# Performance work log

Hardware: AMD Instinct MI355X
Metric: run time of the kernel (lower is better)

Reference implementation:

```python
import jax, jax.numpy as jnp
import numpy as np

D_MODEL = 768
N_HEADS = 12
D_HEAD = D_MODEL // N_HEADS
D_FF = 3072
EPS = 1e-5


def setup_inputs() -> dict:
    key = jax.random.key(0)
    ks = jax.random.split(key, 12)
    s = 0.02
    return {
        "x": jax.random.normal(ks[0], (2, 2048, D_MODEL), dtype=jnp.float32),
        "ln1_g": jnp.ones((D_MODEL,), jnp.float32),
        "ln1_b": jnp.zeros((D_MODEL,), jnp.float32),
        "ln2_g": jnp.ones((D_MODEL,), jnp.float32),
        "ln2_b": jnp.zeros((D_MODEL,), jnp.float32),
        "w_qkv": jax.random.normal(ks[1], (D_MODEL, 3 * D_MODEL), jnp.float32) * s,
        "b_qkv": jnp.zeros((3 * D_MODEL,), jnp.float32),
        "w_out": jax.random.normal(ks[2], (D_MODEL, D_MODEL), jnp.float32) * s,
        "b_out": jnp.zeros((D_MODEL,), jnp.float32),
        "w_fc1": jax.random.normal(ks[3], (D_MODEL, D_FF), jnp.float32) * s,
        "b_fc1": jnp.zeros((D_FF,), jnp.float32),
        "w_fc2": jax.random.normal(ks[4], (D_FF, D_MODEL), jnp.float32) * s,
        "b_fc2": jnp.zeros((D_MODEL,), jnp.float32),
    }


def _layernorm(x, g, b):
    mu = jnp.mean(x, axis=-1, keepdims=True)
    var = jnp.var(x, axis=-1, keepdims=True)
    return (x - mu) * jax.lax.rsqrt(var + EPS) * g + b


def _attention(h, w_qkv, b_qkv, w_out, b_out):
    B, S, _ = h.shape
    qkv = h @ w_qkv + b_qkv  # [B,S,3D]
    qkv = qkv.reshape(B, S, 3, N_HEADS, D_HEAD)
    q, k, v = qkv[:, :, 0], qkv[:, :, 1], qkv[:, :, 2]  # [B,S,H,Dh]
    scale = 1.0 / np.sqrt(D_HEAD).astype(np.float32)
    scores = jnp.einsum("bqhd,bkhd->bhqk", q, k) * scale
    causal = jnp.tril(jnp.ones((S, S), bool))
    scores = jnp.where(causal[None, None], scores, -jnp.inf)
    attn = jax.nn.softmax(scores, axis=-1)
    out = jnp.einsum("bhqk,bkhd->bqhd", attn, v).reshape(B, S, D_MODEL)
    return out @ w_out + b_out


def reference(x, ln1_g, ln1_b, ln2_g, ln2_b, w_qkv, b_qkv, w_out, b_out,
              w_fc1, b_fc1, w_fc2, b_fc2):
    # x = x + Attention(LN1(x))
    x = x + _attention(_layernorm(x, ln1_g, ln1_b), w_qkv, b_qkv, w_out, b_out)
    # x = x + FFN(LN2(x)); GELU is exact (erf) to match torch nn.GELU default
    h = _layernorm(x, ln2_g, ln2_b)
    h = jax.nn.gelu(h @ w_fc1 + b_fc1, approximate=False) @ w_fc2 + b_fc2
    return x + h
```

## Files before the change

### kernel.cpp

```cpp
#include <hip/hip_runtime.h>
#include <hip/hip_bf16.h>

typedef unsigned short u16;
typedef unsigned int u32;
typedef unsigned char u8;
using short8 = __attribute__((ext_vector_type(8))) short;
using short4v = __attribute__((ext_vector_type(4))) short;
using f32x4  = __attribute__((ext_vector_type(4))) float;
using float4v = __attribute__((ext_vector_type(4))) float;

__device__ __forceinline__ u16 f2bf(float f) {
    __hip_bfloat16 h = __float2bfloat16(f);
    union { __hip_bfloat16 h; u16 u; } cv; cv.h = h; return cv.u;
}
__device__ __forceinline__ float bf2f(u16 u) {
    union { u32 u; float f; } cv; cv.u = ((u32)u) << 16; return cv.f;
}
__device__ __forceinline__ u16 f2bf_trunc(float f) {
    union { float f; u32 u; } cv; cv.f = f; return (u16)(cv.u >> 16);
}

__device__ __forceinline__ void gload_lds16(const void* g, void* l) {
    __builtin_amdgcn_global_load_lds(
        (const __attribute__((address_space(1))) u32*)g,
        (__attribute__((address_space(3))) u32*)l, 16, 0, 0);
}

__device__ __forceinline__ int xcd_remap(int flat, int nwg) {
    int q = nwg >> 3, r = nwg & 7;
    int xcd = flat & 7, pos = flat >> 3;
    int start = xcd < r ? xcd * (q + 1) : r * (q + 1) + (xcd - r) * q;
    return start + pos;
}

__global__ __launch_bounds__(256) void transpose_all(const float* __restrict__ Wq,
                                                     const float* __restrict__ Wo,
                                                     const float* __restrict__ Wf1,
                                                     const float* __restrict__ Wf2,
                                                     u16* __restrict__ Tq,
                                                     u16* __restrict__ To,
                                                     u16* __restrict__ Tf1,
                                                     u16* __restrict__ Tf2) {
    __shared__ float tile[32][33];
    int id = blockIdx.x;
    const float* W; u16* Wt; int K, N, local;
    if (id < 1728)      { W = Wq;  Wt = Tq;  K = 768;  N = 2304; local = id; }
    else if (id < 2304) { W = Wo;  Wt = To;  K = 768;  N = 768;  local = id - 1728; }
    else if (id < 4608) { W = Wf1; Wt = Tf1; K = 768;  N = 3072; local = id - 2304; }
    else                { W = Wf2; Wt = Tf2; K = 3072; N = 768;  local = id - 4608; }
    int bx = N >> 5;
    int n0 = (local % bx) * 32, k0 = (local / bx) * 32;
    int tx = threadIdx.x & 31, ty = threadIdx.x >> 5;
    for (int i = 0; i < 4; i++) {
        int k = ty + i * 8;
        tile[k][tx] = W[(long)(k0 + k) * N + n0 + tx];
    }
    __syncthreads();
    for (int i = 0; i < 4; i++) {
        int n = ty + i * 8;
        Wt[(long)(n0 + n) * K + k0 + tx] = f2bf(tile[tx][n]);
    }
}

__global__ __launch_bounds__(256) void transpose_v(const u16* __restrict__ qkv,
                                                   u16* __restrict__ Vt) {
    __shared__ u16 tile[64][72];
    int s0 = blockIdx.x * 64;
    int bh = blockIdx.y;
    int b = bh / 12, h = bh % 12;
    int tid = threadIdx.x;
    const u16* src = qkv + (long)b * 2048 * 2304 + 1536 + h * 64;
    #pragma unroll
    for (int j = 0; j < 2; ++j) {
        int c = tid + j * 256;
        int srow = c >> 3, ch = c & 7;
        *(short8*)&tile[srow][ch * 8] = *(const short8*)(src + (long)(s0 + srow) * 2304 + ch * 8);
    }
    __syncthreads();
    u16* dst = Vt + (long)bh * 64 * 2048 + s0;
    #pragma unroll
    for (int j = 0; j < 2; ++j) {
        int c = tid + j * 256;
        int d = c >> 3, ch = c & 7;
        short8 v;
        #pragma unroll
        for (int e = 0; e < 8; ++e) v[e] = (short)tile[ch * 8 + e][d];
        *(short8*)(dst + (long)d * 2048 + ch * 8) = v;
    }
}

__global__ __launch_bounds__(256) void ln_kernel(const float* __restrict__ x,
                                                 const float* __restrict__ gain,
                                                 const float* __restrict__ beta,
                                                 u16* __restrict__ out) {
    int row = blockIdx.x;
    const float* xr = x + (long)row * 768;
    int tid = threadIdx.x;
    float v[3];
    float s = 0.f, s2 = 0.f;
    for (int j = 0; j < 3; j++) {
        v[j] = xr[tid + 256 * j];
        s += v[j]; s2 += v[j] * v[j];
    }
    for (int off = 32; off; off >>= 1) {
        s  += __shfl_down(s, off);
        s2 += __shfl_down(s2, off);
    }
    __shared__ float ws[8];
    int lane = tid & 63, w = tid >> 6;
    if (lane == 0) { ws[w] = s; ws[4 + w] = s2; }
    __syncthreads();
    s  = ws[0] + ws[1] + ws[2] + ws[3];
    s2 = ws[4] + ws[5] + ws[6] + ws[7];
    float mu  = s * (1.f / 768.f);
    float var = s2 * (1.f / 768.f) - mu * mu;
    float rs  = rsqrtf(var + 1e-5f);
    for (int j = 0; j < 3; j++) {
        int c = tid + 256 * j;
        out[(long)row * 768 + c] = f2bf((v[j] - mu) * rs * gain[c] + beta[c]);
    }
}

template <int EPI>
__global__ __launch_bounds__(256) void gemm_bf16(const u16* __restrict__ A, int lda,
                                                 const u16* __restrict__ Bt, int ldb,
                                                 const float* __restrict__ bias,
                                                 const float* __restrict__ res,
                                                 void* __restrict__ Cout0,
                                                 void* __restrict__ Cout1,
                                                 int M, int N, int K, int nN) {
    __shared__ alignas(16) u16 As[3][128 * 32];
    __shared__ alignas(16) u16 Bs[3][128 * 32];
    int nwg = gridDim.x;
    int wgid = xcd_remap(blockIdx.x, nwg);
    int tN = (wgid % nN) * 128, tM = (wgid / nN) * 128;
    int z = blockIdx.z;
    const u16* Ab = A + (long)z * K;
    const u16* Bb = Bt + (long)z * K;
    void* Cw = z ? Cout1 : Cout0;
    int tid = threadIdx.x;
    int wid = tid >> 6, lane = tid & 63;
    int wm = wid >> 1, wn = wid & 1;
    int g = lane >> 4, r = lane & 15;
    int srow = tid >> 2;
    int scol = tid & 3;

    f32x4 acc[4][4] = {};
    int KT = K >> 5;

    auto stage = [&](int kt, int buf) {
        int k0 = kt << 5;
        u16* ab = As[buf];
        u16* bb = Bs[buf];
        #pragma unroll
        for (int j = 0; j < 2; ++j) {
            int row = j * 64 + srow;
            int slot = scol ^ (row & 3);
            gload_lds16(Ab + (long)(tM + row) * lda + k0 + slot * 8, ab + (j * 64 + wid * 16) * 32);
            gload_lds16(Bb + (long)(tN + row) * ldb + k0 + slot * 8, bb + (j * 64 + wid * 16) * 32);
        }
    };

    stage(0, 0);
    stage(1, 1);
    int sb = 2, cb = 0;
    for (int kt = 0; kt < KT; ++kt) {
        if (kt + 2 < KT) {
            stage(kt + 2, sb);
            if (++sb == 3) sb = 0;
            asm volatile("s_waitcnt vmcnt(8)" ::: "memory");
        } else if (kt + 1 < KT) {
            asm volatile("s_waitcnt vmcnt(4)" ::: "memory");
        } else {
            asm volatile("s_waitcnt vmcnt(0)" ::: "memory");
        }
        __builtin_amdgcn_sched_barrier(0);
        __builtin_amdgcn_s_barrier();
        const u16* ab = As[cb];
        const u16* bb = Bs[cb];
        if (++cb == 3) cb = 0;

        short8 af[4], bf[4];
        #pragma unroll
        for (int mi = 0; mi < 4; ++mi) {
            int row = wm * 64 + mi * 16 + r;
            af[mi] = *(const short8*)(ab + row * 32 + ((g ^ (row & 3)) * 8));
        }
        #pragma unroll
        for (int ni = 0; ni < 4; ++ni) {
            int row = wn * 64 + ni * 16 + r;
            bf[ni] = *(const short8*)(bb + row * 32 + ((g ^ (row & 3)) * 8));
        }
        #pragma unroll
        for (int mi = 0; mi < 4; ++mi)
            #pragma unroll
            for (int ni = 0; ni < 4; ++ni)
                acc[mi][ni] = __builtin_amdgcn_mfma_f32_16x16x32_bf16(af[mi], bf[ni], acc[mi][ni], 0, 0, 0);
        __builtin_amdgcn_s_barrier();
    }

    #pragma unroll
    for (int mi = 0; mi < 4; mi++) {
        #pragma unroll
        for (int ni = 0; ni < 4; ni++) {
            int col = tN + wn * 64 + ni * 16 + r;
            float bv = (EPI == 3) ? 0.f : bias[col];
            #pragma unroll
            for (int reg = 0; reg < 4; reg++) {
                int row = tM + wm * 64 + mi * 16 + g * 4 + reg;
                float v = acc[mi][ni][reg] + bv;
                if (EPI == 1) {
                    v += res[(long)row * N + col];
                    ((float*)Cw)[(long)row * N + col] = v;
                } else if (EPI == 2) {
                    v = 0.5f * v * (1.f + erff(v * 0.70710678118f));
                    ((u16*)Cw)[(long)row * N + col] = f2bf(v);
                } else if (EPI == 3) {
                    ((u16*)Cw)[(long)row * N + col] = f2bf(v);
                } else {
                    ((u16*)Cw)[(long)row * N + col] = f2bf(v);
                }
            }
        }
    }
}

__global__ __launch_bounds__(192) void fc2_combine(const u16* __restrict__ P0,
                                                   const u16* __restrict__ P1,
                                                   const float* __restrict__ bias,
                                                   const float* __restrict__ res,
                                                   float* __restrict__ out) {
    long row = blockIdx.x;
    int c = threadIdx.x * 4;
    long i = row * 768 + c;
    short4v a = *(const short4v*)(P0 + i);
    short4v b = *(const short4v*)(P1 + i);
    float4v bs = *(const float4v*)(bias + c);
    float4v rr = *(const float4v*)(res + i);
    float4v o;
    #pragma unroll
    for (int j = 0; j < 4; ++j)
        o[j] = bf2f((u16)a[j]) + bf2f((u16)b[j]) + bs[j] + rr[j];
    *(float4v*)(out + i) = o;
}

__device__ __constant__ u8 SLOT_QI[40] = {
    15,15,15,15, 14,14,14, 13,13,13, 12,12,12, 11,11,11, 10,10, 9,9, 8,8, 7,7, 6, 5, 4, 3,
    14,10,6,2,  13,9,5,1,  12,8,4,0 };
__device__ __constant__ u8 SLOT_C[40] = {
    0,1,2,3, 0,1,2, 0,1,2, 0,1,2, 0,1,2, 0,1, 0,1, 0,1, 0,1, 0, 0, 0, 0,
    3,2,1,0, 3,2,1,0, 3,2,1,0 };

__global__ __launch_bounds__(256) void attn_kernel(const u16* __restrict__ qkv,
                                                   const u16* __restrict__ Vt,
                                                   u16* __restrict__ Opart,
                                                   float* __restrict__ Ml) {
    __shared__ alignas(16) u16 Ks[2 * 64 * 64];
    __shared__ alignas(16) u16 Vs[2 * 64 * 64];
    __shared__ alignas(16) u16 Ps[4 * 16 * 64];
    int flat = blockIdx.x;
    int s = flat / 24, bh = flat % 24;
    int qi = SLOT_QI[s], c = SLOT_C[s];
    int b = bh / 12, h = bh % 12;
    int tid = threadIdx.x;
    int w = tid >> 6, lane = tid & 63;
    int g = lane >> 4, r = lane & 15;
    int qt0 = qi * 128;
    int qw0 = qt0 + w * 32;
    int kvbase = c * 512;
    int nit = (c < (qi >> 2)) ? 8 : (2 * (qi & 3) + 2);
    const u16* base = qkv + (long)b * 2048 * 2304;
    const u16* Qb = base + h * 64;
    const u16* Kb = base + 768 + h * 64;
    const u16* Vtb = Vt + (long)bh * 64 * 2048;

    const float SC = 0.125f * 1.44269504f;
    short8 qf[2][2];
    #pragma unroll
    for (int fi = 0; fi < 2; ++fi) {
        const u16* qrow = Qb + (long)(qw0 + fi * 16 + r) * 2304;
        qf[fi][0] = *(const short8*)(qrow + 8 * g);
        qf[fi][1] = *(const short8*)(qrow + 32 + 8 * g);
        #pragma unroll
        for (int kh = 0; kh < 2; ++kh)
            #pragma unroll
            for (int j = 0; j < 8; ++j)
                qf[fi][kh][j] = (short)f2bf(bf2f((u16)qf[fi][kh][j]) * SC);
    }

    f32x4 oacc[2][4] = {};
    float mrow[2][4], psum[2][4];
    #pragma unroll
    for (int fi = 0; fi < 2; ++fi)
        #pragma unroll
        for (int i = 0; i < 4; i++) { mrow[fi][i] = 8.0f; psum[fi][i] = 0.f; }

    auto stage = [&](int kt) {
        int kv0 = kvbase + kt * 64;
        u16* kb = Ks + (kt & 1) * 4096;
        u16* vb = Vs + (kt & 1) * 4096;
        #pragma unroll
        for (int j = 0; j < 2; ++j) {
            int cc = w * 128 + j * 64 + lane;
            int row = cc >> 3;
            int slot = (cc & 7) ^ (row & 7);
            gload_lds16(Kb + (long)(kv0 + row) * 2304 + slot * 8, kb + (w * 128 + j * 64) * 8);
            gload_lds16(Vtb + (long)row * 2048 + kv0 + slot * 8, vb + (w * 128 + j * 64) * 8);
        }
    };

    stage(0);
    for (int kt = 0; kt < nit; ++kt) {
        int kv0 = kvbase + kt * 64;
        if (kt + 1 < nit) {
            stage(kt + 1);
            asm volatile("s_waitcnt vmcnt(4)" ::: "memory");
        } else {
            asm volatile("s_waitcnt vmcnt(0)" ::: "memory");
        }
        __builtin_amdgcn_sched_barrier(0);
        __builtin_amdgcn_s_barrier();
        const u16* kb = Ks + (kt & 1) * 4096;
        const u16* vb = Vs + (kt & 1) * 4096;

        bool act0 = kv0 <= qw0 + 15;
        bool act1 = kv0 <= qw0 + 31;

        f32x4 sc[2][4] = {};
        if (act1) {
            __builtin_amdgcn_s_setprio(1);
            #pragma unroll
            for (int nt = 0; nt < 4; ++nt)
                #pragma unroll
                for (int kh = 0; kh < 2; ++kh) {
                    short8 bk = *(const short8*)(kb + (nt * 16 + r) * 64 + ((kh * 32 + g * 8) ^ ((r & 7) << 3)));
                    sc[1][nt] = __builtin_amdgcn_mfma_f32_16x16x32_bf16(qf[1][kh], bk, sc[1][nt], 0, 0, 0);
                    if (act0)
                        sc[0][nt] = __builtin_amdgcn_mfma_f32_16x16x32_bf16(qf[0][kh], bk, sc[0][nt], 0, 0, 0);
                }
            __builtin_amdgcn_s_setprio(0);

            #pragma unroll
            for (int fi = 0; fi < 2; ++fi) {
                if (fi == 0 && !act0) continue;
                if ((kv0 + 63) > (qw0 + fi * 16)) {
                    #pragma unroll
                    for (int nt = 0; nt < 4; ++nt)
                        #pragma unroll
                        for (int reg = 0; reg < 4; ++reg)
                            if ((kv0 + nt * 16 + r) > (qw0 + fi * 16 + g * 4 + reg))
                                sc[fi][nt][reg] = -1e30f;
                }
            }

            float tl[2][4];
            bool need = false;
            #pragma unroll
            for (int fi = 0; fi < 2; ++fi) {
                if (fi == 0 && !act0) continue;
                #pragma unroll
                for (int reg = 0; reg < 4; ++reg) {
                    tl[fi][reg] = fmaxf(fmaxf(sc[fi][0][reg], sc[fi][1][reg]),
                                        fmaxf(sc[fi][2][reg], sc[fi][3][reg]));
                    need = need || (tl[fi][reg] > mrow[fi][reg] + 8.f);
                }
            }
            if (__any(need)) {
                #pragma unroll
                for (int fi = 0; fi < 2; ++fi) {
                    if (fi == 0 && !act0) continue;
                    #pragma unroll
                    for (int reg = 0; reg < 4; ++reg) {
                        float rm = tl[fi][reg];
                        #pragma unroll
                        for (int off = 1; off < 16; off <<= 1)
                            rm = fmaxf(rm, __shfl_xor(rm, off));
                        float mnew = fmaxf(mrow[fi][reg], rm);
                        float alpha = exp2f(mrow[fi][reg] - mnew);
                        mrow[fi][reg] = mnew;
                        psum[fi][reg] *= alpha;
                        #pragma unroll
                        for (int dt = 0; dt < 4; ++dt) oacc[fi][dt][reg] *= alpha;
                    }
                }
            }

            short8 pf[2][2];
            u16* Pw = Ps + w * 16 * 64;
            #pragma unroll
            for (int fi = 0; fi < 2; ++fi) {
                if (fi == 0 && !act0) continue;
                #pragma unroll
                for (int nt = 0; nt < 4; ++nt)
                    #pragma unroll
                    for (int reg = 0; reg < 4; ++reg) {
                        float p = exp2f(sc[fi][nt][reg] - mrow[fi][reg]);
                        psum[fi][reg] += p;
                        int row = g * 4 + reg;
                        Pw[row * 64 + ((nt * 16 + r) ^ ((row & 7) << 3))] = f2bf_trunc(p);
                    }
                pf[fi][0] = *(const short8*)(Pw + r * 64 + ((g * 8) ^ ((r & 7) << 3)));
                pf[fi][1] = *(const short8*)(Pw + r * 64 + ((32 + g * 8) ^ ((r & 7) << 3)));
            }

            __builtin_amdgcn_s_setprio(1);
            #pragma unroll
            for (int dt = 0; dt < 4; ++dt)
                #pragma unroll
                for (int kc = 0; kc < 2; ++kc) {
                    short8 vf = *(const short8*)(vb + (dt * 16 + r) * 64 + ((kc * 32 + g * 8) ^ ((r & 7) << 3)));
                    oacc[1][dt] = __builtin_amdgcn_mfma_f32_16x16x32_bf16(pf[1][kc], vf, oacc[1][dt], 0, 0, 0);
                    if (act0)
                        oacc[0][dt] = __builtin_amdgcn_mfma_f32_16x16x32_bf16(pf[0][kc], vf, oacc[0][dt], 0, 0, 0);
                }
            __builtin_amdgcn_s_setprio(0);
        }
        __builtin_amdgcn_s_barrier();
    }

    float lrow[2][4];
    #pragma unroll
    for (int fi = 0; fi < 2; ++fi)
        #pragma unroll
        for (int reg = 0; reg < 4; ++reg) {
            float l = psum[fi][reg];
            #pragma unroll
            for (int off = 1; off < 16; off <<= 1)
                l += __shfl_xor(l, off);
            lrow[fi][reg] = l;
        }

    long pbase = ((long)c * 24 + bh) * 2048;
    #pragma unroll
    for (int fi = 0; fi < 2; ++fi)
        #pragma unroll
        for (int dt = 0; dt < 4; ++dt)
            #pragma unroll
            for (int reg = 0; reg < 4; ++reg) {
                int q = qw0 + fi * 16 + g * 4 + reg;
                int d = dt * 16 + r;
                Opart[(pbase + q) * 64 + d] = f2bf(oacc[fi][dt][reg]);
            }
    if (r == 0) {
        #pragma unroll
        for (int fi = 0; fi < 2; ++fi)
            #pragma unroll
            for (int reg = 0; reg < 4; ++reg) {
                int q = qw0 + fi * 16 + g * 4 + reg;
                Ml[(pbase + q) * 2]     = mrow[fi][reg];
                Ml[(pbase + q) * 2 + 1] = lrow[fi][reg];
            }
    }
}

__global__ __launch_bounds__(256) void attn_combine(const u16* __restrict__ Opart,
                                                    const float* __restrict__ Ml,
                                                    u16* __restrict__ Ob) {
    int bh = blockIdx.y;
    int b = bh / 12, h = bh % 12;
    int q = blockIdx.x * 4 + (threadIdx.x >> 6);
    int d = threadIdx.x & 63;
    int qi = q >> 7;
    int nact = (qi >> 2) + 1;
    float mv[4], lv[4];
    float M = -1e30f;
    for (int c = 0; c < nact; ++c) {
        long base = ((long)c * 24 + bh) * 2048 + q;
        mv[c] = Ml[base * 2];
        lv[c] = Ml[base * 2 + 1];
        M = fmaxf(M, mv[c]);
    }
    float denom = 0.f, val = 0.f;
    for (int c = 0; c < nact; ++c) {
        float wgt = exp2f(mv[c] - M);
        denom += lv[c] * wgt;
        val += wgt * bf2f(Opart[(((long)c * 24 + bh) * 2048 + q) * 64 + d]);
    }
    Ob[((long)b * 2048 + q) * 768 + h * 64 + d] = f2bf(val / denom);
}

extern "C" void kernel_launch(void* const* d_in, const int* in_sizes, int n_in,
                              void* d_out, int out_size, void* d_ws, size_t ws_size,
                              hipStream_t stream) {
    const float* x     = (const float*)d_in[0];
    const float* ln1_g = (const float*)d_in[1];
    const float* ln1_b = (const float*)d_in[2];
    const float* ln2_g = (const float*)d_in[3];
    const float* ln2_b = (const float*)d_in[4];
    const float* w_qkv = (const float*)d_in[5];
    const float* b_qkv = (const float*)d_in[6];
    const float* w_out = (const float*)d_in[7];
    const float* b_out = (const float*)d_in[8];
    const float* w_fc1 = (const float*)d_in[9];
    const float* b_fc1 = (const float*)d_in[10];
    const float* w_fc2 = (const float*)d_in[11];
    const float* b_fc2 = (const float*)d_in[12];

    char* ws = (char*)d_ws;
    size_t off = 0;
    auto alloc = [&](size_t bytes) { void* p = ws + off; off += (bytes + 255) & ~255ULL; return p; };
    u16* h1    = (u16*)alloc(4096UL * 768 * 2);
    u16* WqkvT = (u16*)alloc(2304UL * 768 * 2);
    u16* WoutT = (u16*)alloc(768UL * 768 * 2);
    u16* Wfc1T = (u16*)alloc(3072UL * 768 * 2);
    u16* Wfc2T = (u16*)alloc(768UL * 3072 * 2);
    u16* qkvb  = (u16*)alloc(4096UL * 2304 * 2);
    u16* Vtb   = (u16*)alloc(24UL * 64 * 2048 * 2);
    u16* Ob    = (u16*)alloc(4096UL * 768 * 2);
    float* x2  = (float*)alloc(4096UL * 768 * 4);
    char* pool = (char*)alloc(4096UL * 768 * 2 + 4096UL * 3072 * 2);
    u16* h2      = (u16*)pool;
    u16* gbuf    = (u16*)(pool + 4096UL * 768 * 2);
    u16* Opart   = (u16*)pool;
    float* Ml    = (float*)(pool + 4UL * 24 * 2048 * 64 * 2);
    u16* P0 = (u16*)qkvb;
    u16* P1 = (u16*)h1;

    transpose_all<<<dim3(6912), 256, 0, stream>>>(w_qkv, w_out, w_fc1, w_fc2,
                                                  WqkvT, WoutT, Wfc1T, Wfc2T);

    ln_kernel<<<4096, 256, 0, stream>>>(x, ln1_g, ln1_b, h1);
    gemm_bf16<0><<<dim3(576, 1, 1), 256, 0, stream>>>(h1, 768, WqkvT, 768, b_qkv, nullptr, qkvb, nullptr, 4096, 2304, 768, 18);
    transpose_v<<<dim3(32, 24), 256, 0, stream>>>(qkvb, Vtb);
    attn_kernel<<<dim3(960), 256, 0, stream>>>(qkvb, Vtb, Opart, Ml);
    attn_combine<<<dim3(512, 24), 256, 0, stream>>>(Opart, Ml, Ob);
    gemm_bf16<1><<<dim3(192, 1, 1), 256, 0, stream>>>(Ob, 768, WoutT, 768, b_out, x, x2, nullptr, 4096, 768, 768, 6);
    ln_kernel<<<4096, 256, 0, stream>>>(x2, ln2_g, ln2_b, h2);
    gemm_bf16<2><<<dim3(768, 1, 1), 256, 0, stream>>>(h2, 768, Wfc1T, 768, b_fc1, nullptr, gbuf, nullptr, 4096, 3072, 768, 24);
    gemm_bf16<3><<<dim3(192, 1, 2), 256, 0, stream>>>(gbuf, 3072, Wfc2T, 3072, nullptr, nullptr, P0, P1, 4096, 768, 1536, 6);
    fc2_combine<<<4096, 192, 0, stream>>>(P0, P1, b_fc2, x2, (float*)d_out);
}
```

Baseline: 206.9 us.

## Merge weight transpose with LN1 and split FC2 K into four partials

Folds the first layernorm into the weight-transpose launch as extra blocks, which removes one kernel launch and lets both run concurrently. The FC2 GEMM's split-K goes from 2 to 4 slices, giving 768 workgroups instead of 384 for better CU occupancy. The combine kernel now sums four bf16 partials, which adds memory traffic and extra bf16 rounding error. Vtb and Ob are reused as partial buffers.

```diff
diff --git a/kernel.cpp b/kernel.cpp
--- a/kernel.cpp
+++ b/kernel.cpp
@@ -33,32 +33,65 @@
     return start + pos;
 }
 
-__global__ __launch_bounds__(256) void transpose_all(const float* __restrict__ Wq,
-                                                     const float* __restrict__ Wo,
-                                                     const float* __restrict__ Wf1,
-                                                     const float* __restrict__ Wf2,
-                                                     u16* __restrict__ Tq,
-                                                     u16* __restrict__ To,
-                                                     u16* __restrict__ Tf1,
-                                                     u16* __restrict__ Tf2) {
+__global__ __launch_bounds__(256) void prep_kernel(const float* __restrict__ Wq,
+                                                   const float* __restrict__ Wo,
+                                                   const float* __restrict__ Wf1,
+                                                   const float* __restrict__ Wf2,
+                                                   u16* __restrict__ Tq,
+                                                   u16* __restrict__ To,
+                                                   u16* __restrict__ Tf1,
+                                                   u16* __restrict__ Tf2,
+                                                   const float* __restrict__ x,
+                                                   const float* __restrict__ gain,
+                                                   const float* __restrict__ beta,
+                                                   u16* __restrict__ h1) {
     __shared__ float tile[32][33];
+    __shared__ float ws[8];
     int id = blockIdx.x;
-    const float* W; u16* Wt; int K, N, local;
-    if (id < 1728)      { W = Wq;  Wt = Tq;  K = 768;  N = 2304; local = id; }
-    else if (id < 2304) { W = Wo;  Wt = To;  K = 768;  N = 768;  local = id - 1728; }
-    else if (id < 4608) { W = Wf1; Wt = Tf1; K = 768;  N = 3072; local = id - 2304; }
-    else                { W = Wf2; Wt = Tf2; K = 3072; N = 768;  local = id - 4608; }
-    int bx = N >> 5;
-    int n0 = (local % bx) * 32, k0 = (local / bx) * 32;
-    int tx = threadIdx.x & 31, ty = threadIdx.x >> 5;
-    for (int i = 0; i < 4; i++) {
-        int k = ty + i * 8;
-        tile[k][tx] = W[(long)(k0 + k) * N + n0 + tx];
-    }
-    __syncthreads();
-    for (int i = 0; i < 4; i++) {
-        int n = ty + i * 8;
-        Wt[(long)(n0 + n) * K + k0 + tx] = f2bf(tile[tx][n]);
+    if (id < 6912) {
+        const float* W; u16* Wt; int K, N, local;
+        if (id < 1728)      { W = Wq;  Wt = Tq;  K = 768;  N = 2304; local = id; }
+        else if (id < 2304) { W = Wo;  Wt = To;  K = 768;  N = 768;  local = id - 1728; }
+        else if (id < 4608) { W = Wf1; Wt = Tf1; K = 768;  N = 3072; local = id - 2304; }
+        else                { W = Wf2; Wt = Tf2; K = 3072; N = 768;  local = id - 4608; }
+        int bx = N >> 5;
+        int n0 = (local % bx) * 32, k0 = (local / bx) * 32;
+        int tx = threadIdx.x & 31, ty = threadIdx.x >> 5;
+        for (int i = 0; i < 4; i++) {
+            int k = ty + i * 8;
+            tile[k][tx] = W[(long)(k0 + k) * N + n0 + tx];
+        }
+        __syncthreads();
+        for (int i = 0; i < 4; i++) {
+            int n = ty + i * 8;
+            Wt[(long)(n0 + n) * K + k0 + tx] = f2bf(tile[tx][n]);
+        }
+    } else {
+        int row = id - 6912;
+        const float* xr = x + (long)row * 768;
+        int tid = threadIdx.x;
+        float v[3];
+        float s = 0.f, s2 = 0.f;
+        for (int j = 0; j < 3; j++) {
+            v[j] = xr[tid + 256 * j];
+            s += v[j]; s2 += v[j] * v[j];
+        }
+        for (int off = 32; off; off >>= 1) {
+            s  += __shfl_down(s, off);
+            s2 += __shfl_down(s2, off);
+        }
+        int lane = tid & 63, w = tid >> 6;
+        if (lane == 0) { ws[w] = s; ws[4 + w] = s2; }
+        __syncthreads();
+        s  = ws[0] + ws[1] + ws[2] + ws[3];
+        s2 = ws[4] + ws[5] + ws[6] + ws[7];
+        float mu  = s * (1.f / 768.f);
+        float var = s2 * (1.f / 768.f) - mu * mu;
+        float rs  = rsqrtf(var + 1e-5f);
+        for (int j = 0; j < 3; j++) {
+            int c = tid + 256 * j;
+            h1[(long)row * 768 + c] = f2bf((v[j] - mu) * rs * gain[c] + beta[c]);
+        }
     }
 }
 
@@ -128,6 +161,8 @@
                                                  const float* __restrict__ res,
                                                  void* __restrict__ Cout0,
                                                  void* __restrict__ Cout1,
+                                                 void* __restrict__ Cout2,
+                                                 void* __restrict__ Cout3,
                                                  int M, int N, int K, int nN) {
     __shared__ alignas(16) u16 As[3][128 * 32];
     __shared__ alignas(16) u16 Bs[3][128 * 32];
@@ -137,7 +172,7 @@
     int z = blockIdx.z;
     const u16* Ab = A + (long)z * K;
     const u16* Bb = Bt + (long)z * K;
-    void* Cw = z ? Cout1 : Cout0;
+    void* Cw = (z == 0) ? Cout0 : (z == 1) ? Cout1 : (z == 2) ? Cout2 : Cout3;
     int tid = threadIdx.x;
     int wid = tid >> 6, lane = tid & 63;
     int wm = wid >> 1, wn = wid & 1;
@@ -215,8 +250,6 @@
                 } else if (EPI == 2) {
                     v = 0.5f * v * (1.f + erff(v * 0.70710678118f));
                     ((u16*)Cw)[(long)row * N + col] = f2bf(v);
-                } else if (EPI == 3) {
-                    ((u16*)Cw)[(long)row * N + col] = f2bf(v);
                 } else {
                     ((u16*)Cw)[(long)row * N + col] = f2bf(v);
                 }
@@ -225,22 +258,26 @@
     }
 }
 
-__global__ __launch_bounds__(192) void fc2_combine(const u16* __restrict__ P0,
-                                                   const u16* __restrict__ P1,
-                                                   const float* __restrict__ bias,
-                                                   const float* __restrict__ res,
-                                                   float* __restrict__ out) {
+__global__ __launch_bounds__(192) void fc2_combine4(const u16* __restrict__ P0,
+                                                    const u16* __restrict__ P1,
+                                                    const u16* __restrict__ P2,
+                                                    const u16* __restrict__ P3,
+                                                    const float* __restrict__ bias,
+                                                    const float* __restrict__ res,
+                                                    float* __restrict__ out) {
     long row = blockIdx.x;
     int c = threadIdx.x * 4;
     long i = row * 768 + c;
     short4v a = *(const short4v*)(P0 + i);
     short4v b = *(const short4v*)(P1 + i);
+    short4v d = *(const short4v*)(P2 + i);
+    short4v e = *(const short4v*)(P3 + i);
     float4v bs = *(const float4v*)(bias + c);
     float4v rr = *(const float4v*)(res + i);
     float4v o;
     #pragma unroll
     for (int j = 0; j < 4; ++j)
-        o[j] = bf2f((u16)a[j]) + bf2f((u16)b[j]) + bs[j] + rr[j];
+        o[j] = (bf2f((u16)a[j]) + bf2f((u16)b[j])) + (bf2f((u16)d[j]) + bf2f((u16)e[j])) + bs[j] + rr[j];
     *(float4v*)(out + i) = o;
 }
 
@@ -515,18 +552,19 @@
     float* Ml    = (float*)(pool + 4UL * 24 * 2048 * 64 * 2);
     u16* P0 = (u16*)qkvb;
     u16* P1 = (u16*)h1;
-
-    transpose_all<<<dim3(6912), 256, 0, stream>>>(w_qkv, w_out, w_fc1, w_fc2,
-                                                  WqkvT, WoutT, Wfc1T, Wfc2T);
-
-    ln_kernel<<<4096, 256, 0, stream>>>(x, ln1_g, ln1_b, h1);
-    gemm_bf16<0><<<dim3(576, 1, 1), 256, 0, stream>>>(h1, 768, WqkvT, 768, b_qkv, nullptr, qkvb, nullptr, 4096, 2304, 768, 18);
+    u16* P2 = (u16*)Vtb;
+    u16* P3 = (u16*)Ob;
+
+    prep_kernel<<<dim3(11008), 256, 0, stream>>>(w_qkv, w_out, w_fc1, w_fc2,
+                                                 WqkvT, WoutT, Wfc1T, Wfc2T,
+                                                 x, ln1_g, ln1_b, h1);
+    gemm_bf16<0><<<dim3(576, 1, 1), 256, 0, stream>>>(h1, 768, WqkvT, 768, b_qkv, nullptr, qkvb, nullptr, nullptr, nullptr, 4096, 2304, 768, 18);
     transpose_v<<<dim3(32, 24), 256, 0, stream>>>(qkvb, Vtb);
     attn_kernel<<<dim3(960), 256, 0, stream>>>(qkvb, Vtb, Opart, Ml);
     attn_combine<<<dim3(512, 24), 256, 0, stream>>>(Opart, Ml, Ob);
-    gemm_bf16<1><<<dim3(192, 1, 1), 256, 0, stream>>>(Ob, 768, WoutT, 768, b_out, x, x2, nullptr, 4096, 768, 768, 6);
+    gemm_bf16<1><<<dim3(192, 1, 1), 256, 0, stream>>>(Ob, 768, WoutT, 768, b_out, x, x2, nullptr, nullptr, nullptr, 4096, 768, 768, 6);
     ln_kernel<<<4096, 256, 0, stream>>>(x2, ln2_g, ln2_b, h2);
-    gemm_bf16<2><<<dim3(768, 1, 1), 256, 0, stream>>>(h2, 768, Wfc1T, 768, b_fc1, nullptr, gbuf, nullptr, 4096, 3072, 768, 24);
-    gemm_bf16<3><<<dim3(192, 1, 2), 256, 0, stream>>>(gbuf, 3072, Wfc2T, 3072, nullptr, nullptr, P0, P1, 4096, 768, 1536, 6);
-    fc2_combine<<<4096, 192, 0, stream>>>(P0, P1, b_fc2, x2, (float*)d_out);
-}
+    gemm_bf16<2><<<dim3(768, 1, 1), 256, 0, stream>>>(h2, 768, Wfc1T, 768, b_fc1, nullptr, gbuf, nullptr, nullptr, nullptr, 4096, 3072, 768, 24);
+    gemm_bf16<3><<<dim3(192, 1, 4), 256, 0, stream>>>(gbuf, 3072, Wfc2T, 3072, nullptr, nullptr, P0, P1, P2, P3, 4096, 768, 768, 6);
+    fc2_combine4<<<4096, 192, 0, stream>>>(P0, P1, P2, P3, b_fc2, x2, (float*)d_out);
+}
```

After: 201.6 us. 1.03x faster.
